# Kernel optimization log

Measured on AMD Instinct MI355X. Metric: run time of the kernel, lower is better.

The kernel has to match this reference:

```python
import jax, jax.numpy as jnp
import numpy as np

N = 100000     # nodes
H = 128        # hidden_channels == in_channels
OUT = 64       # out_channels
L = 3          # num_layers=4 -> num_layers-1 Layer modules
E = 1_600_000  # unique undirected edges (avg degree 16)
BN_EPS = 1e-5


def _make_edges():
    # Unique undirected edges, no self-loops -> dense symmetric adjacency in the
    # original module is exactly this edge set symmetrized.
    rng = np.random.default_rng(0)
    i = rng.integers(0, N, 1_700_000)
    j = rng.integers(0, N, 1_700_000)
    m = i != j
    i, j = i[m], j[m]
    lo, hi = np.minimum(i, j), np.maximum(i, j)
    pairs = np.unique(lo.astype(np.int64) * N + hi)[:E]
    lo = (pairs // N).astype(np.int32)
    hi = (pairs % N).astype(np.int32)
    src = jnp.asarray(np.concatenate([lo, hi]))  # [2E] directed
    dst = jnp.asarray(np.concatenate([hi, lo]))
    return src, dst


def setup_inputs() -> dict:
    key = jax.random.key(0)
    ks = jax.random.split(key, 24)
    nrm = lambda k, s: (jax.random.normal(k, s, dtype=jnp.float32) * 0.05)
    src, dst = _make_edges()
    return {
        "x": jax.random.normal(ks[0], (N, H), dtype=jnp.float32),
        "src": src,
        "dst": dst,
        # per-Layer MLP(in=H, hidden=H, out=H): Linear->ReLU->Linear, stacked over L
        "layer_W1": nrm(ks[1], (L, H, H)),
        "layer_b1": nrm(ks[2], (L, H)),
        "layer_W2": nrm(ks[3], (L, H, H)),
        "layer_b2": nrm(ks[4], (L, H)),
        # BatchNorm1d (eval mode: running stats)
        "bn_gamma": 1.0 + nrm(ks[5], (L, H)),
        "bn_beta": nrm(ks[6], (L, H)),
        "bn_mean": nrm(ks[7], (L, H)),
        "bn_var": jax.random.uniform(ks[8], (L, H), jnp.float32, 0.5, 1.5),
        # single shared GRUCell(H, H)
        "gru_Wih": nrm(ks[9], (3 * H, H)),
        "gru_Whh": nrm(ks[10], (3 * H, H)),
        "gru_bih": nrm(ks[11], (3 * H,)),
        "gru_bhh": nrm(ks[12], (3 * H,)),
        # mlp_last: MLP(H, H, OUT)
        "last_W1": nrm(ks[13], (H, H)),
        "last_b1": nrm(ks[14], (H,)),
        "last_W2": nrm(ks[15], (OUT, H)),
        "last_b2": nrm(ks[16], (OUT,)),
    }


def reference(x, src, dst, layer_W1, layer_b1, layer_W2, layer_b2,
              bn_gamma, bn_beta, bn_mean, bn_var,
              gru_Wih, gru_Whh, gru_bih, gru_bhh,
              last_W1, last_b1, last_W2, last_b2):
    n = x.shape[0]
    deg = jax.ops.segment_sum(jnp.ones(src.shape[0], x.dtype), dst, num_segments=n)
    inv_deg = (1.0 / jnp.maximum(deg, 1.0))[:, None]  # isolated nodes -> 0 agg
    h = jnp.zeros((n, H), x.dtype)
    for l in range(L):
        agg = jax.ops.segment_sum(x[src], dst, num_segments=n) * inv_deg  # mean over neighbors
        c = x + agg
        c = jnp.maximum(c @ layer_W1[l].T + layer_b1[l], 0.0) @ layer_W2[l].T + layer_b2[l]
        c = bn_gamma[l] * (c - bn_mean[l]) * jax.lax.rsqrt(bn_var[l] + BN_EPS) + bn_beta[l]
        # F.dropout(training=False) is identity
        gi = c @ gru_Wih.T + gru_bih  # [n, 3H]
        gh = h @ gru_Whh.T + gru_bhh
        r = jax.nn.sigmoid(gi[:, :H] + gh[:, :H])
        z = jax.nn.sigmoid(gi[:, H:2 * H] + gh[:, H:2 * H])
        nst = jnp.tanh(gi[:, 2 * H:] + r * gh[:, 2 * H:])
        h = (1.0 - z) * nst + z * h
        x = h
    return jnp.maximum(x @ last_W1.T + last_b1, 0.0) @ last_W2.T + last_b2
```

## Files before the change

### kernel.cpp

```cpp
#include <hip/hip_runtime.h>
#include <hip/hip_bf16.h>
#include <stdint.h>

typedef __bf16 bf16;
typedef __bf16 bf16x8 __attribute__((ext_vector_type(8)));
typedef float f32x4 __attribute__((ext_vector_type(4)));
typedef uint32_t u32x4 __attribute__((ext_vector_type(4)));

#define HD 128
#define LDP (HD + 8)
#define NTPB 4
#define MFMA __builtin_amdgcn_mfma_f32_16x16x32_bf16

__device__ inline float bflo(uint32_t u){ return __uint_as_float(u << 16); }
__device__ inline float bfhi(uint32_t u){ return __uint_as_float(u & 0xffff0000u); }
__device__ inline uint32_t packbf(float a, float b){
    bf16 x = (bf16)a, y = (bf16)b;
    uint16_t ux = __builtin_bit_cast(uint16_t, x), uy = __builtin_bit_cast(uint16_t, y);
    return (uint32_t)ux | ((uint32_t)uy << 16);
}
__device__ inline bf16x8 ldb8(const bf16* p){ return *(const bf16x8*)p; }
__device__ inline float sigm(float x){ return 1.f / (1.f + __expf(-x)); }
__device__ inline float tanh_fast(float x){ float t = __expf(-2.f * x); return (1.f - t) / (1.f + t); }

__global__ void k_cvt(const float* __restrict__ in, bf16* __restrict__ out, int n){
    int i = blockIdx.x * 256 + threadIdx.x;
    if (i < n) out[i] = (bf16)in[i];
}

__global__ void k_bound(const int* __restrict__ dstB, int E, int* __restrict__ rows2, int n){
    int v = blockIdx.x * 256 + threadIdx.x;
    if (v > n) return;
    int lo = 0, hi = E;
    while (lo < hi){ int mid = (lo + hi) >> 1; if (dstB[mid] < v) lo = mid + 1; else hi = mid; }
    rows2[v] = lo;
}

__global__ void k_count(const int* __restrict__ dst, int* __restrict__ deg, int ne){
    int i = blockIdx.x * 256 + threadIdx.x;
    if (i < ne) atomicAdd(&deg[dst[i]], 1);
}

__global__ void k_scan1(const int* __restrict__ deg, int* __restrict__ rows,
                        int* __restrict__ bsum, int n){
    __shared__ int lds[256];
    int b = blockIdx.x, tid = threadIdx.x;
    int i0 = b * 1024 + tid * 4;
    int v[4]; int s = 0;
#pragma unroll
    for (int j = 0; j < 4; ++j){ int idx = i0 + j; v[j] = (idx < n) ? deg[idx] : 0; s += v[j]; }
    lds[tid] = s; __syncthreads();
    int acc = s;
    for (int off = 1; off < 256; off <<= 1){
        int add = (tid >= off) ? lds[tid - off] : 0;
        __syncthreads();
        acc += add; lds[tid] = acc;
        __syncthreads();
    }
    int run = acc - s;
#pragma unroll
    for (int j = 0; j < 4; ++j){ int idx = i0 + j; if (idx < n) rows[idx] = run; run += v[j]; }
    if (tid == 255) bsum[b] = acc;
}

__global__ void k_scan2(int* __restrict__ bsum, int nb){
    __shared__ int lds[128];
    int tid = threadIdx.x;
    int v = (tid < nb) ? bsum[tid] : 0;
    lds[tid] = v; __syncthreads();
    int acc = v;
    for (int off = 1; off < 128; off <<= 1){
        int add = (tid >= off) ? lds[tid - off] : 0;
        __syncthreads();
        acc += add; lds[tid] = acc;
        __syncthreads();
    }
    if (tid < nb) bsum[tid] = acc - v;
}

__global__ void k_scan3(int* __restrict__ rows, const int* __restrict__ bsum, int n, int total){
    int i = blockIdx.x * 256 + threadIdx.x;
    if (i < n) rows[i] += bsum[i >> 10];
    if (i == n) rows[n] = total;
}

__global__ void k_fill(const int* __restrict__ src, const int* __restrict__ dst,
                       int* __restrict__ cur, int* __restrict__ col, int ne){
    int i = blockIdx.x * 256 + threadIdx.x;
    if (i < ne){ int p = atomicAdd(&cur[dst[i]], 1); col[p] = src[i]; }
}

__global__ __launch_bounds__(256) void k_gather(
    const bf16* __restrict__ curx,
    const int* __restrict__ srcB, const int* __restrict__ rows2,
    const int* __restrict__ colB, const int* __restrict__ rowsB,
    bf16* __restrict__ cout, int n)
{
    int wid = threadIdx.x >> 6, lane = threadIdx.x & 63;
    int v = blockIdx.x * 4 + wid;
    if (v >= n) return;
    int grp = lane >> 3, sl = lane & 7;
    int a0 = rows2[v], a1 = rows2[v + 1];
    int b0 = rowsB[v], b1 = rowsB[v + 1];
    int deg = (a1 - a0) + (b1 - b0);
    float inv = (deg > 0) ? 1.f / (float)deg : 0.f;

    const u32x4* base = (const u32x4*)curx;
    float acc[16];
#pragma unroll
    for (int k = 0; k < 16; ++k) acc[k] = 0.f;

    for (int j = a0 + grp; j < a1; j += 8){
        int nb = srcB[j];
        u32x4 q0 = base[(size_t)nb * 16 + sl];
        u32x4 q1 = base[(size_t)nb * 16 + 8 + sl];
#pragma unroll
        for (int k = 0; k < 4; ++k){
            acc[2*k]   += bflo(q0[k]); acc[2*k+1]   += bfhi(q0[k]);
            acc[8+2*k] += bflo(q1[k]); acc[8+2*k+1] += bfhi(q1[k]);
        }
    }
    for (int j = b0 + grp; j < b1; j += 8){
        int nb = colB[j];
        u32x4 q0 = base[(size_t)nb * 16 + sl];
        u32x4 q1 = base[(size_t)nb * 16 + 8 + sl];
#pragma unroll
        for (int k = 0; k < 4; ++k){
            acc[2*k]   += bflo(q0[k]); acc[2*k+1]   += bfhi(q0[k]);
            acc[8+2*k] += bflo(q1[k]); acc[8+2*k+1] += bfhi(q1[k]);
        }
    }
#pragma unroll
    for (int k = 0; k < 16; ++k){
        acc[k] += __shfl_xor(acc[k], 8);
        acc[k] += __shfl_xor(acc[k], 16);
        acc[k] += __shfl_xor(acc[k], 32);
    }
    if (grp == 0){
        u32x4 x0 = base[(size_t)v * 16 + sl];
        u32x4 x1 = base[(size_t)v * 16 + 8 + sl];
        u32x4 o0, o1;
#pragma unroll
        for (int k = 0; k < 4; ++k){
            o0[k] = packbf(bflo(x0[k]) + acc[2*k] * inv,   bfhi(x0[k]) + acc[2*k+1] * inv);
            o1[k] = packbf(bflo(x1[k]) + acc[8+2*k] * inv, bfhi(x1[k]) + acc[8+2*k+1] * inv);
        }
        ((u32x4*)cout)[(size_t)v * 16 + sl]     = o0;
        ((u32x4*)cout)[(size_t)v * 16 + 8 + sl] = o1;
    }
}

__global__ __launch_bounds__(256, 2) void k_layer(
    const bf16* __restrict__ cin, bf16* __restrict__ h,
    const bf16* __restrict__ W1, const float* __restrict__ b1,
    const bf16* __restrict__ W2, const float* __restrict__ b2,
    const float* __restrict__ gm, const float* __restrict__ bt,
    const float* __restrict__ mu, const float* __restrict__ vr,
    const bf16* __restrict__ Wih, const bf16* __restrict__ Whh,
    const float* __restrict__ bih, const float* __restrict__ bhh)
{
    __shared__ __align__(16) char wsm[49152];
    __shared__ __align__(16) bf16 act[4][4096];
    int wid = threadIdx.x >> 6, lane = threadIdx.x & 63;
    int r0 = blockIdx.x * 128 + wid * 32;
    int rA = lane & 15, u = lane >> 4, ko = u * 8;

    auto swz = [](uint32_t off)->uint32_t { return off ^ (((off >> 8) & 7) << 4); };
    auto gload = [&](const char* gsrc, uint32_t ldsoff){
        __builtin_amdgcn_global_load_lds(
            (const __attribute__((address_space(1))) void*)gsrc,
            (__attribute__((address_space(3))) void*)(wsm + ldsoff), 16, 0, 0);
    };
    for (int i = wid; i < 32; i += 4){
        uint32_t off = (uint32_t)i * 1024 + (uint32_t)lane * 16;
        gload((const char*)W1 + swz(off), (uint32_t)i * 1024);
    }

    bf16x8 a[2][4], ah[2][4];
#pragma unroll
    for (int m = 0; m < 2; ++m){
        const bf16* ap = cin + (size_t)(r0 + m*16 + rA) * HD + ko;
        const bf16* hp = h   + (size_t)(r0 + m*16 + rA) * HD + ko;
#pragma unroll
        for (int kk = 0; kk < 4; ++kk){ a[m][kk] = ldb8(ap + kk*32); ah[m][kk] = ldb8(hp + kk*32); }
    }

    auto ldw = [&](int slot, int kk)->bf16x8 {
        uint32_t b = (uint32_t)rA*256 + (uint32_t)u*16 + (uint32_t)kk*64;
        b ^= ((b >> 8) & 7) << 4;
        return *(const bf16x8*)(wsm + slot*4096 + b);
    };
    auto actw = [&](int r, int c, bf16 val){
        uint32_t b = (uint32_t)r*256 + (uint32_t)c*2;
        b ^= ((b >> 8) & 7) << 4;
        *(bf16*)((char*)act[wid] + b) = val;
    };
    auto actr = [&](int r, int kk)->bf16x8 {
        uint32_t b = (uint32_t)r*256 + (uint32_t)(ko + kk*32)*2;
        b ^= ((b >> 8) & 7) << 4;
        return *(const bf16x8*)((char*)act[wid] + b);
    };

    __syncthreads();

    for (int i = wid; i < 16; i += 4){
        uint32_t off = (uint32_t)i * 1024 + (uint32_t)lane * 16;
        gload((const char*)W2 + swz(off), 8*4096u + (uint32_t)i * 1024);
    }
#pragma unroll
    for (int t = 0; t < 8; ++t){
        f32x4 c0 = {0,0,0,0}, c1 = {0,0,0,0};
#pragma unroll
        for (int kk = 0; kk < 4; ++kk){
            bf16x8 wb = ldw(t, kk);
            c0 = MFMA(a[0][kk], wb, c0, 0, 0, 0);
            c1 = MFMA(a[1][kk], wb, c1, 0, 0, 0);
        }
        int c = t*16 + rA;
        float bias = b1[c];
#pragma unroll
        for (int j = 0; j < 4; ++j){
            actw(u*4 + j,      c, (bf16)fmaxf(c0[j] + bias, 0.f));
            actw(16 + u*4 + j, c, (bf16)fmaxf(c1[j] + bias, 0.f));
        }
    }
    __syncthreads();

    for (int i = wid; i < 16; i += 4){
        uint32_t off = 16384u + (uint32_t)i * 1024 + (uint32_t)lane * 16;
        gload((const char*)W2 + swz(off), (uint32_t)i * 1024);
    }
    bf16x8 a2[2][4];
#pragma unroll
    for (int m = 0; m < 2; ++m)
#pragma unroll
        for (int kk = 0; kk < 4; ++kk) a2[m][kk] = actr(m*16 + rA, kk);

    auto g2step = [&](int t, int slot){
        f32x4 c0 = {0,0,0,0}, c1 = {0,0,0,0};
#pragma unroll
        for (int kk = 0; kk < 4; ++kk){
            bf16x8 wb = ldw(slot, kk);
            c0 = MFMA(a2[0][kk], wb, c0, 0, 0, 0);
            c1 = MFMA(a2[1][kk], wb, c1, 0, 0, 0);
        }
        int c = t*16 + rA;
        float s = gm[c] * rsqrtf(vr[c] + 1e-5f);
        float o = bt[c] - mu[c] * s;
        float bias = b2[c];
#pragma unroll
        for (int j = 0; j < 4; ++j){
            actw(u*4 + j,      c, (bf16)((c0[j] + bias) * s + o));
            actw(16 + u*4 + j, c, (bf16)((c1[j] + bias) * s + o));
        }
    };
#pragma unroll
    for (int t = 0; t < 4; ++t) g2step(t, 8 + t);
    __syncthreads();

    auto stageGRU = [&](int t){
        uint32_t sb = (t & 1) ? 10u : 4u;
        for (int i = wid; i < 24; i += 4){
            int p = i >> 2, s = i & 3;
            int g = p >> 1, m = p & 1;
            const char* Wsrc = (const char*)(m ? Whh : Wih) + (size_t)g*32768 + (size_t)t*4096;
            uint32_t slot = sb + (uint32_t)p; if (slot >= 12) slot -= 12;
            uint32_t off = (uint32_t)s * 1024 + (uint32_t)lane * 16;
            gload(Wsrc + swz(off), slot*4096 + (uint32_t)s * 1024);
        }
    };
    stageGRU(0);
#pragma unroll
    for (int t = 4; t < 8; ++t) g2step(t, t - 4);
    __syncthreads();

    bf16x8 ac[2][4];
#pragma unroll
    for (int m = 0; m < 2; ++m)
#pragma unroll
        for (int kk = 0; kk < 4; ++kk) ac[m][kk] = actr(m*16 + rA, kk);

#pragma unroll
    for (int t = 0; t < 8; ++t){
        if (t < 7) stageGRU(t + 1);
        uint32_t sb = (t & 1) ? 10u : 4u;
        int s0 = sb, s1 = sb+1, s2 = sb+2, s3 = sb+3, s4 = sb+4, s5 = sb+5;
        if (s2 >= 12) s2 -= 12; if (s3 >= 12) s3 -= 12;
        if (s4 >= 12) s4 -= 12; if (s5 >= 12) s5 -= 12;
        if (s1 >= 12) s1 -= 12;
        int c = t*16 + rA;
        float hold[8];
#pragma unroll
        for (int j = 0; j < 4; ++j){
            hold[j]   = (float)h[(size_t)(r0 + u*4 + j) * HD + c];
            hold[4+j] = (float)h[(size_t)(r0 + 16 + u*4 + j) * HD + c];
        }
        f32x4 rr0={0,0,0,0}, rr1={0,0,0,0}, zz0={0,0,0,0}, zz1={0,0,0,0};
        f32x4 gi0={0,0,0,0}, gi1={0,0,0,0}, gh0={0,0,0,0}, gh1={0,0,0,0};
#pragma unroll
        for (int kk = 0; kk < 4; ++kk){
            bf16x8 Bri = ldw(s0, kk), Brh = ldw(s1, kk);
            bf16x8 Bzi = ldw(s2, kk), Bzh = ldw(s3, kk);
            bf16x8 Bni = ldw(s4, kk), Bnh = ldw(s5, kk);
            rr0 = MFMA(ac[0][kk], Bri, rr0, 0, 0, 0);
            rr1 = MFMA(ac[1][kk], Bri, rr1, 0, 0, 0);
            rr0 = MFMA(ah[0][kk], Brh, rr0, 0, 0, 0);
            rr1 = MFMA(ah[1][kk], Brh, rr1, 0, 0, 0);
            zz0 = MFMA(ac[0][kk], Bzi, zz0, 0, 0, 0);
            zz1 = MFMA(ac[1][kk], Bzi, zz1, 0, 0, 0);
            zz0 = MFMA(ah[0][kk], Bzh, zz0, 0, 0, 0);
            zz1 = MFMA(ah[1][kk], Bzh, zz1, 0, 0, 0);
            gi0 = MFMA(ac[0][kk], Bni, gi0, 0, 0, 0);
            gi1 = MFMA(ac[1][kk], Bni, gi1, 0, 0, 0);
            gh0 = MFMA(ah[0][kk], Bnh, gh0, 0, 0, 0);
            gh1 = MFMA(ah[1][kk], Bnh, gh1, 0, 0, 0);
        }
        float br = bih[c] + bhh[c];
        float bz = bih[c + 128] + bhh[c + 128];
        float bin = bih[c + 256], bhn = bhh[c + 256];
#pragma unroll
        for (int j = 0; j < 4; ++j){
            size_t i0 = (size_t)(r0 + u*4 + j) * HD + c;
            size_t i1 = (size_t)(r0 + 16 + u*4 + j) * HD + c;
            float rg0 = sigm(rr0[j] + br), rg1 = sigm(rr1[j] + br);
            float zg0 = sigm(zz0[j] + bz), zg1 = sigm(zz1[j] + bz);
            float ng0 = tanh_fast(gi0[j] + bin + rg0 * (gh0[j] + bhn));
            float ng1 = tanh_fast(gi1[j] + bin + rg1 * (gh1[j] + bhn));
            h[i0] = (bf16)((1.f - zg0) * ng0 + zg0 * hold[j]);
            h[i1] = (bf16)((1.f - zg1) * ng1 + zg1 * hold[4+j]);
        }
        __syncthreads();
    }
}

__global__ __launch_bounds__(256) void k_final(
    const bf16* __restrict__ hin, const bf16* __restrict__ W1, const float* __restrict__ b1,
    const bf16* __restrict__ W2, const float* __restrict__ b2,
    float* __restrict__ out, int nTiles)
{
    __shared__ bf16 lds[NTPB][16][LDP];
    int wid = threadIdx.x >> 6, lane = threadIdx.x & 63;
    int tile = blockIdx.x * NTPB + wid;
    if (tile >= nTiles) return;
    int r0 = tile * 16;
    int rA = lane & 15, u = lane >> 4, ko = u * 8;

    bf16x8 a[4];
    const bf16* ap = hin + (size_t)(r0 + rA) * HD + ko;
#pragma unroll
    for (int kk = 0; kk < 4; ++kk) a[kk] = ldb8(ap + kk * 32);

#pragma unroll
    for (int t = 0; t < 8; ++t){
        f32x4 acc = {0.f, 0.f, 0.f, 0.f};
        int c = t * 16 + rA;
        const bf16* bp = W1 + (size_t)c * HD + ko;
#pragma unroll
        for (int kk = 0; kk < 4; ++kk)
            acc = MFMA(a[kk], ldb8(bp + kk * 32), acc, 0, 0, 0);
        float bias = b1[c];
#pragma unroll
        for (int j = 0; j < 4; ++j){
            float v = fmaxf(acc[j] + bias, 0.f);
            lds[wid][u * 4 + j][c] = (bf16)v;
        }
    }
    __threadfence_block();
    bf16x8 a2[4];
    const bf16* lp = &lds[wid][rA][ko];
#pragma unroll
    for (int kk = 0; kk < 4; ++kk) a2[kk] = ldb8(lp + kk * 32);

#pragma unroll
    for (int t = 0; t < 4; ++t){
        f32x4 acc = {0.f, 0.f, 0.f, 0.f};
        int c = t * 16 + rA;
        const bf16* bp = W2 + (size_t)c * HD + ko;
#pragma unroll
        for (int kk = 0; kk < 4; ++kk)
            acc = MFMA(a2[kk], ldb8(bp + kk * 32), acc, 0, 0, 0);
        float bias = b2[c];
#pragma unroll
        for (int j = 0; j < 4; ++j)
            out[(size_t)(r0 + u * 4 + j) * 64 + c] = acc[j] + bias;
    }
}

extern "C" void kernel_launch(void* const* d_in, const int* in_sizes, int n_in,
                              void* d_out, int out_size, void* d_ws, size_t ws_size,
                              hipStream_t stream)
{
    const float* x    = (const float*)d_in[0];
    const int*   src  = (const int*)d_in[1];
    const int*   dst  = (const int*)d_in[2];
    const float* lW1  = (const float*)d_in[3];
    const float* lb1  = (const float*)d_in[4];
    const float* lW2  = (const float*)d_in[5];
    const float* lb2  = (const float*)d_in[6];
    const float* gmm  = (const float*)d_in[7];
    const float* bta  = (const float*)d_in[8];
    const float* mun  = (const float*)d_in[9];
    const float* vrr  = (const float*)d_in[10];
    const float* Wih  = (const float*)d_in[11];
    const float* Whh  = (const float*)d_in[12];
    const float* bih  = (const float*)d_in[13];
    const float* bhh  = (const float*)d_in[14];
    const float* fW1  = (const float*)d_in[15];
    const float* fb1  = (const float*)d_in[16];
    const float* fW2  = (const float*)d_in[17];
    const float* fb2  = (const float*)d_in[18];

    int n  = in_sizes[0] / HD;
    int ne = in_sizes[1];
    int E  = ne / 2;
    int L  = in_sizes[3] / (HD * HD);
    int nPad = (n + 127) & ~127;

    char* w = (char*)d_ws;
    auto alloc = [&](size_t bytes) -> char* {
        char* p = w; w += (bytes + 255) & ~(size_t)255; return p;
    };
    bf16* xbf  = (bf16*)alloc((size_t)nPad * HD * 2);
    bf16* hbf  = (bf16*)alloc((size_t)nPad * HD * 2);
    bf16* cin  = (bf16*)alloc((size_t)nPad * HD * 2);
    bf16* W1b  = (bf16*)alloc((size_t)L * HD * HD * 2);
    bf16* W2b  = (bf16*)alloc((size_t)L * HD * HD * 2);
    bf16* Wib  = (bf16*)alloc((size_t)3 * HD * HD * 2);
    bf16* Whb  = (bf16*)alloc((size_t)3 * HD * HD * 2);
    bf16* fW1b = (bf16*)alloc((size_t)HD * HD * 2);
    bf16* fW2b = (bf16*)alloc((size_t)64 * HD * 2);
    int*  degB = (int*)alloc((size_t)n * 4);
    int*  rowsB= (int*)alloc((size_t)(n + 1) * 4);
    int*  rows2= (int*)alloc((size_t)(n + 1) * 4);
    int*  bsum = (int*)alloc(512);
    int*  curB = (int*)alloc((size_t)n * 4);
    int*  colB = (int*)alloc((size_t)E * 4);

    auto cvt = [&](const float* i, bf16* o, int cnt){
        k_cvt<<<(cnt + 255) / 256, 256, 0, stream>>>(i, o, cnt);
    };
    cvt(x,   xbf,  n * HD);
    cvt(lW1, W1b,  L * HD * HD);
    cvt(lW2, W2b,  L * HD * HD);
    cvt(Wih, Wib,  3 * HD * HD);
    cvt(Whh, Whb,  3 * HD * HD);
    cvt(fW1, fW1b, HD * HD);
    cvt(fW2, fW2b, 64 * HD);

    hipMemsetAsync(degB, 0, (size_t)n * 4, stream);
    hipMemsetAsync(hbf, 0, (size_t)nPad * HD * 2, stream);

    k_bound<<<(n + 1 + 255) / 256, 256, 0, stream>>>(dst + E, E, rows2, n);
    k_count<<<(E + 255) / 256, 256, 0, stream>>>(dst, degB, E);
    int nb = (n + 1023) / 1024;
    k_scan1<<<nb, 256, 0, stream>>>(degB, rowsB, bsum, n);
    k_scan2<<<1, 128, 0, stream>>>(bsum, nb);
    k_scan3<<<(n + 1 + 255) / 256, 256, 0, stream>>>(rowsB, bsum, n, E);
    hipMemcpyAsync(curB, rowsB, (size_t)n * 4, hipMemcpyDeviceToDevice, stream);
    k_fill<<<(E + 255) / 256, 256, 0, stream>>>(src, dst, curB, colB, E);

    int gL = nPad / 128;
    int nT16 = (n + 15) / 16;
    int gF = (nT16 + NTPB - 1) / NTPB;

    const bf16* curp = xbf;
    for (int l = 0; l < L; ++l){
        k_gather<<<(n + 3) / 4, 256, 0, stream>>>(curp, src + E, rows2, colB, rowsB, cin, n);
        k_layer<<<gL, 256, 0, stream>>>(cin, hbf,
            W1b + (size_t)l * HD * HD, lb1 + l * HD,
            W2b + (size_t)l * HD * HD, lb2 + l * HD,
            gmm + l * HD, bta + l * HD, mun + l * HD, vrr + l * HD,
            Wib, Whb, bih, bhh);
        curp = hbf;
    }
    k_final<<<gF, 256, 0, stream>>>(hbf, fW1b, fb1, fW2b, fb2, (float*)d_out, nT16);
}
```

Baseline: 819.7 us.

## Split fused layer kernel into persistent MLP and column-split GRU kernels

After: 1.076 ms. +31.3%, slower.

```diff
diff --git a/kernel.cpp b/kernel.cpp
--- a/kernel.cpp
+++ b/kernel.cpp
@@ -22,6 +22,7 @@
 __device__ inline bf16x8 ldb8(const bf16* p){ return *(const bf16x8*)p; }
 __device__ inline float sigm(float x){ return 1.f / (1.f + __expf(-x)); }
 __device__ inline float tanh_fast(float x){ float t = __expf(-2.f * x); return (1.f - t) / (1.f + t); }
+__device__ inline uint32_t swz(uint32_t b){ return b ^ (((b >> 8) & 7u) << 4); }
 
 __global__ void k_cvt(const float* __restrict__ in, bf16* __restrict__ out, int n){
     int i = blockIdx.x * 256 + threadIdx.x;
@@ -150,186 +151,165 @@
     }
 }
 
-__global__ __launch_bounds__(256, 2) void k_layer(
-    const bf16* __restrict__ cin, bf16* __restrict__ h,
-    const bf16* __restrict__ W1, const float* __restrict__ b1,
-    const bf16* __restrict__ W2, const float* __restrict__ b2,
+__global__ __launch_bounds__(512, 2) void k_mlp(
+    bf16* __restrict__ cio,
+    const bf16* __restrict__ W1g, const float* __restrict__ b1,
+    const bf16* __restrict__ W2g, const float* __restrict__ b2,
     const float* __restrict__ gm, const float* __restrict__ bt,
-    const float* __restrict__ mu, const float* __restrict__ vr,
+    const float* __restrict__ mu, const float* __restrict__ vr, int nT128)
+{
+    __shared__ __align__(16) char wsm[65536];
+    __shared__ __align__(16) char actm[32768];
+    int tid = threadIdx.x, wid = tid >> 6, lane = tid & 63;
+    int rA = lane & 15, u = lane >> 4, ko = u * 8;
+
+#pragma unroll
+    for (int i = 0; i < 8; ++i){
+        int c = i * 8 + wid;
+        uint32_t o = (uint32_t)c * 1024;
+        const char* base = (c < 32) ? (const char*)W1g : (const char*)W2g;
+        uint32_t po = (o & 32767u) + (uint32_t)lane * 16;
+        __builtin_amdgcn_global_load_lds(
+            (const __attribute__((address_space(1))) void*)(base + swz(po)),
+            (__attribute__((address_space(3))) void*)(wsm + o), 16, 0, 0);
+    }
+    __syncthreads();
+
+    char* act = actm + wid * 4096;
+    auto ldw = [&](uint32_t regionOff, int t, int kk)->bf16x8 {
+        uint32_t b = regionOff + (uint32_t)(t*16 + rA)*256 + (uint32_t)u*16 + (uint32_t)kk*64;
+        return *(const bf16x8*)(wsm + swz(b));
+    };
+    auto actw = [&](int r, int c, bf16 val){
+        uint32_t b = (uint32_t)r*256 + (uint32_t)c*2;
+        *(bf16*)(act + swz(b)) = val;
+    };
+    auto actr = [&](int r, int kk)->bf16x8 {
+        uint32_t b = (uint32_t)r*256 + (uint32_t)(ko + kk*32)*2;
+        return *(const bf16x8*)(act + swz(b));
+    };
+
+    for (int t = blockIdx.x; t < nT128; t += gridDim.x){
+        int r0 = t * 128 + wid * 16;
+        bf16x8 a[4];
+        const bf16* ap = cio + (size_t)(r0 + rA) * HD + ko;
+#pragma unroll
+        for (int kk = 0; kk < 4; ++kk) a[kk] = ldb8(ap + kk * 32);
+
+#pragma unroll
+        for (int tt = 0; tt < 8; ++tt){
+            f32x4 acc = {0,0,0,0};
+#pragma unroll
+            for (int kk = 0; kk < 4; ++kk)
+                acc = MFMA(a[kk], ldw(0, tt, kk), acc, 0, 0, 0);
+            int c = tt*16 + rA;
+            float bias = b1[c];
+#pragma unroll
+            for (int j = 0; j < 4; ++j)
+                actw(u*4 + j, c, (bf16)fmaxf(acc[j] + bias, 0.f));
+        }
+        __threadfence_block();
+        bf16x8 a2[4];
+#pragma unroll
+        for (int kk = 0; kk < 4; ++kk) a2[kk] = actr(rA, kk);
+
+#pragma unroll
+        for (int tt = 0; tt < 8; ++tt){
+            f32x4 acc = {0,0,0,0};
+#pragma unroll
+            for (int kk = 0; kk < 4; ++kk)
+                acc = MFMA(a2[kk], ldw(32768u, tt, kk), acc, 0, 0, 0);
+            int c = tt*16 + rA;
+            float s = gm[c] * rsqrtf(vr[c] + 1e-5f);
+            float o = bt[c] - mu[c] * s;
+            float bias = b2[c];
+#pragma unroll
+            for (int j = 0; j < 4; ++j)
+                cio[(size_t)(r0 + u*4 + j) * HD + c] = (bf16)((acc[j] + bias) * s + o);
+        }
+        __threadfence_block();
+    }
+}
+
+__global__ __launch_bounds__(256, 3) void k_gru(
+    const bf16* __restrict__ cbn, const bf16* __restrict__ hOld, bf16* __restrict__ hNew,
     const bf16* __restrict__ Wih, const bf16* __restrict__ Whh,
-    const float* __restrict__ bih, const float* __restrict__ bhh)
+    const float* __restrict__ bih, const float* __restrict__ bhh, int nT128)
 {
     __shared__ __align__(16) char wsm[49152];
-    __shared__ __align__(16) bf16 act[4][4096];
-    int wid = threadIdx.x >> 6, lane = threadIdx.x & 63;
-    int r0 = blockIdx.x * 128 + wid * 32;
+    int tid = threadIdx.x, wid = tid >> 6, lane = tid & 63;
+    int ug = blockIdx.x & 3;
     int rA = lane & 15, u = lane >> 4, ko = u * 8;
 
-    auto swz = [](uint32_t off)->uint32_t { return off ^ (((off >> 8) & 7) << 4); };
-    auto gload = [&](const char* gsrc, uint32_t ldsoff){
+#pragma unroll
+    for (int i = 0; i < 12; ++i){
+        int c = i * 4 + wid;
+        uint32_t o = (uint32_t)c * 1024;
+        int p = o >> 13;
+        int g = p >> 1, m = p & 1;
+        const char* base = (const char*)(m ? Whh : Wih) + ((size_t)(g * 128 + ug * 32)) * 256;
+        uint32_t po = (o & 8191u) + (uint32_t)lane * 16;
         __builtin_amdgcn_global_load_lds(
-            (const __attribute__((address_space(1))) void*)gsrc,
-            (__attribute__((address_space(3))) void*)(wsm + ldsoff), 16, 0, 0);
-    };
-    for (int i = wid; i < 32; i += 4){
-        uint32_t off = (uint32_t)i * 1024 + (uint32_t)lane * 16;
-        gload((const char*)W1 + swz(off), (uint32_t)i * 1024);
-    }
-
-    bf16x8 a[2][4], ah[2][4];
-#pragma unroll
-    for (int m = 0; m < 2; ++m){
-        const bf16* ap = cin + (size_t)(r0 + m*16 + rA) * HD + ko;
-        const bf16* hp = h   + (size_t)(r0 + m*16 + rA) * HD + ko;
-#pragma unroll
-        for (int kk = 0; kk < 4; ++kk){ a[m][kk] = ldb8(ap + kk*32); ah[m][kk] = ldb8(hp + kk*32); }
-    }
-
-    auto ldw = [&](int slot, int kk)->bf16x8 {
-        uint32_t b = (uint32_t)rA*256 + (uint32_t)u*16 + (uint32_t)kk*64;
-        b ^= ((b >> 8) & 7) << 4;
-        return *(const bf16x8*)(wsm + slot*4096 + b);
-    };
-    auto actw = [&](int r, int c, bf16 val){
-        uint32_t b = (uint32_t)r*256 + (uint32_t)c*2;
-        b ^= ((b >> 8) & 7) << 4;
-        *(bf16*)((char*)act[wid] + b) = val;
-    };
-    auto actr = [&](int r, int kk)->bf16x8 {
-        uint32_t b = (uint32_t)r*256 + (uint32_t)(ko + kk*32)*2;
-        b ^= ((b >> 8) & 7) << 4;
-        return *(const bf16x8*)((char*)act[wid] + b);
-    };
-
+            (const __attribute__((address_space(1))) void*)(base + swz(po)),
+            (__attribute__((address_space(3))) void*)(wsm + o), 16, 0, 0);
+    }
     __syncthreads();
 
-    for (int i = wid; i < 16; i += 4){
-        uint32_t off = (uint32_t)i * 1024 + (uint32_t)lane * 16;
-        gload((const char*)W2 + swz(off), 8*4096u + (uint32_t)i * 1024);
-    }
-#pragma unroll
-    for (int t = 0; t < 8; ++t){
-        f32x4 c0 = {0,0,0,0}, c1 = {0,0,0,0};
-#pragma unroll
-        for (int kk = 0; kk < 4; ++kk){
-            bf16x8 wb = ldw(t, kk);
-            c0 = MFMA(a[0][kk], wb, c0, 0, 0, 0);
-            c1 = MFMA(a[1][kk], wb, c1, 0, 0, 0);
-        }
-        int c = t*16 + rA;
-        float bias = b1[c];
-#pragma unroll
-        for (int j = 0; j < 4; ++j){
-            actw(u*4 + j,      c, (bf16)fmaxf(c0[j] + bias, 0.f));
-            actw(16 + u*4 + j, c, (bf16)fmaxf(c1[j] + bias, 0.f));
-        }
-    }
-    __syncthreads();
-
-    for (int i = wid; i < 16; i += 4){
-        uint32_t off = 16384u + (uint32_t)i * 1024 + (uint32_t)lane * 16;
-        gload((const char*)W2 + swz(off), (uint32_t)i * 1024);
-    }
-    bf16x8 a2[2][4];
-#pragma unroll
-    for (int m = 0; m < 2; ++m)
-#pragma unroll
-        for (int kk = 0; kk < 4; ++kk) a2[m][kk] = actr(m*16 + rA, kk);
-
-    auto g2step = [&](int t, int slot){
-        f32x4 c0 = {0,0,0,0}, c1 = {0,0,0,0};
-#pragma unroll
-        for (int kk = 0; kk < 4; ++kk){
-            bf16x8 wb = ldw(slot, kk);
-            c0 = MFMA(a2[0][kk], wb, c0, 0, 0, 0);
-            c1 = MFMA(a2[1][kk], wb, c1, 0, 0, 0);
-        }
-        int c = t*16 + rA;
-        float s = gm[c] * rsqrtf(vr[c] + 1e-5f);
-        float o = bt[c] - mu[c] * s;
-        float bias = b2[c];
-#pragma unroll
-        for (int j = 0; j < 4; ++j){
-            actw(u*4 + j,      c, (bf16)((c0[j] + bias) * s + o));
-            actw(16 + u*4 + j, c, (bf16)((c1[j] + bias) * s + o));
-        }
-    };
-#pragma unroll
-    for (int t = 0; t < 4; ++t) g2step(t, 8 + t);
-    __syncthreads();
-
-    auto stageGRU = [&](int t){
-        uint32_t sb = (t & 1) ? 10u : 4u;
-        for (int i = wid; i < 24; i += 4){
-            int p = i >> 2, s = i & 3;
-            int g = p >> 1, m = p & 1;
-            const char* Wsrc = (const char*)(m ? Whh : Wih) + (size_t)g*32768 + (size_t)t*4096;
-            uint32_t slot = sb + (uint32_t)p; if (slot >= 12) slot -= 12;
-            uint32_t off = (uint32_t)s * 1024 + (uint32_t)lane * 16;
-            gload(Wsrc + swz(off), slot*4096 + (uint32_t)s * 1024);
-        }
-    };
-    stageGRU(0);
-#pragma unroll
-    for (int t = 4; t < 8; ++t) g2step(t, t - 4);
-    __syncthreads();
-
-    bf16x8 ac[2][4];
-#pragma unroll
-    for (int m = 0; m < 2; ++m)
-#pragma unroll
-        for (int kk = 0; kk < 4; ++kk) ac[m][kk] = actr(m*16 + rA, kk);
-
-#pragma unroll
-    for (int t = 0; t < 8; ++t){
-        if (t < 7) stageGRU(t + 1);
-        uint32_t sb = (t & 1) ? 10u : 4u;
-        int s0 = sb, s1 = sb+1, s2 = sb+2, s3 = sb+3, s4 = sb+4, s5 = sb+5;
-        if (s2 >= 12) s2 -= 12; if (s3 >= 12) s3 -= 12;
-        if (s4 >= 12) s4 -= 12; if (s5 >= 12) s5 -= 12;
-        if (s1 >= 12) s1 -= 12;
-        int c = t*16 + rA;
-        float hold[8];
-#pragma unroll
-        for (int j = 0; j < 4; ++j){
-            hold[j]   = (float)h[(size_t)(r0 + u*4 + j) * HD + c];
-            hold[4+j] = (float)h[(size_t)(r0 + 16 + u*4 + j) * HD + c];
-        }
-        f32x4 rr0={0,0,0,0}, rr1={0,0,0,0}, zz0={0,0,0,0}, zz1={0,0,0,0};
-        f32x4 gi0={0,0,0,0}, gi1={0,0,0,0}, gh0={0,0,0,0}, gh1={0,0,0,0};
-#pragma unroll
-        for (int kk = 0; kk < 4; ++kk){
-            bf16x8 Bri = ldw(s0, kk), Brh = ldw(s1, kk);
-            bf16x8 Bzi = ldw(s2, kk), Bzh = ldw(s3, kk);
-            bf16x8 Bni = ldw(s4, kk), Bnh = ldw(s5, kk);
-            rr0 = MFMA(ac[0][kk], Bri, rr0, 0, 0, 0);
-            rr1 = MFMA(ac[1][kk], Bri, rr1, 0, 0, 0);
-            rr0 = MFMA(ah[0][kk], Brh, rr0, 0, 0, 0);
-            rr1 = MFMA(ah[1][kk], Brh, rr1, 0, 0, 0);
-            zz0 = MFMA(ac[0][kk], Bzi, zz0, 0, 0, 0);
-            zz1 = MFMA(ac[1][kk], Bzi, zz1, 0, 0, 0);
-            zz0 = MFMA(ah[0][kk], Bzh, zz0, 0, 0, 0);
-            zz1 = MFMA(ah[1][kk], Bzh, zz1, 0, 0, 0);
-            gi0 = MFMA(ac[0][kk], Bni, gi0, 0, 0, 0);
-            gi1 = MFMA(ac[1][kk], Bni, gi1, 0, 0, 0);
-            gh0 = MFMA(ah[0][kk], Bnh, gh0, 0, 0, 0);
-            gh1 = MFMA(ah[1][kk], Bnh, gh1, 0, 0, 0);
-        }
-        float br = bih[c] + bhh[c];
-        float bz = bih[c + 128] + bhh[c + 128];
-        float bin = bih[c + 256], bhn = bhh[c + 256];
-#pragma unroll
-        for (int j = 0; j < 4; ++j){
-            size_t i0 = (size_t)(r0 + u*4 + j) * HD + c;
-            size_t i1 = (size_t)(r0 + 16 + u*4 + j) * HD + c;
-            float rg0 = sigm(rr0[j] + br), rg1 = sigm(rr1[j] + br);
-            float zg0 = sigm(zz0[j] + bz), zg1 = sigm(zz1[j] + bz);
-            float ng0 = tanh_fast(gi0[j] + bin + rg0 * (gh0[j] + bhn));
-            float ng1 = tanh_fast(gi1[j] + bin + rg1 * (gh1[j] + bhn));
-            h[i0] = (bf16)((1.f - zg0) * ng0 + zg0 * hold[j]);
-            h[i1] = (bf16)((1.f - zg1) * ng1 + zg1 * hold[4+j]);
-        }
-        __syncthreads();
+    auto ldw = [&](int p, int ct, int kk)->bf16x8 {
+        uint32_t b = (uint32_t)p*8192 + (uint32_t)(ct*16 + rA)*256 + (uint32_t)u*16 + (uint32_t)kk*64;
+        return *(const bf16x8*)(wsm + swz(b));
+    };
+
+    int nB = (int)(gridDim.x >> 2);
+    for (int t = (int)(blockIdx.x >> 2); t < nT128; t += nB){
+        int r0 = t * 128 + wid * 32;
+        bf16x8 ac[2][4], ah[2][4];
+#pragma unroll
+        for (int m = 0; m < 2; ++m){
+            const bf16* cp = cbn  + (size_t)(r0 + m*16 + rA) * HD + ko;
+            const bf16* hp = hOld + (size_t)(r0 + m*16 + rA) * HD + ko;
+#pragma unroll
+            for (int kk = 0; kk < 4; ++kk){ ac[m][kk] = ldb8(cp + kk*32); ah[m][kk] = ldb8(hp + kk*32); }
+        }
+#pragma unroll
+        for (int ct = 0; ct < 2; ++ct){
+            f32x4 rr0={0,0,0,0}, rr1={0,0,0,0}, zz0={0,0,0,0}, zz1={0,0,0,0};
+            f32x4 gi0={0,0,0,0}, gi1={0,0,0,0}, gh0={0,0,0,0}, gh1={0,0,0,0};
+#pragma unroll
+            for (int kk = 0; kk < 4; ++kk){
+                bf16x8 Bri = ldw(0, ct, kk), Brh = ldw(1, ct, kk);
+                bf16x8 Bzi = ldw(2, ct, kk), Bzh = ldw(3, ct, kk);
+                bf16x8 Bni = ldw(4, ct, kk), Bnh = ldw(5, ct, kk);
+                rr0 = MFMA(ac[0][kk], Bri, rr0, 0, 0, 0);
+                rr1 = MFMA(ac[1][kk], Bri, rr1, 0, 0, 0);
+                rr0 = MFMA(ah[0][kk], Brh, rr0, 0, 0, 0);
+                rr1 = MFMA(ah[1][kk], Brh, rr1, 0, 0, 0);
+                zz0 = MFMA(ac[0][kk], Bzi, zz0, 0, 0, 0);
+                zz1 = MFMA(ac[1][kk], Bzi, zz1, 0, 0, 0);
+                zz0 = MFMA(ah[0][kk], Bzh, zz0, 0, 0, 0);
+                zz1 = MFMA(ah[1][kk], Bzh, zz1, 0, 0, 0);
+                gi0 = MFMA(ac[0][kk], Bni, gi0, 0, 0, 0);
+                gi1 = MFMA(ac[1][kk], Bni, gi1, 0, 0, 0);
+                gh0 = MFMA(ah[0][kk], Bnh, gh0, 0, 0, 0);
+                gh1 = MFMA(ah[1][kk], Bnh, gh1, 0, 0, 0);
+            }
+            int c = ug * 32 + ct * 16 + rA;
+            float br = bih[c] + bhh[c];
+            float bz = bih[c + 128] + bhh[c + 128];
+            float bin = bih[c + 256], bhn = bhh[c + 256];
+#pragma unroll
+            for (int j = 0; j < 4; ++j){
+                size_t i0 = (size_t)(r0 + u*4 + j) * HD + c;
+                size_t i1 = (size_t)(r0 + 16 + u*4 + j) * HD + c;
+                float h0 = (float)hOld[i0], h1 = (float)hOld[i1];
+                float rg0 = sigm(rr0[j] + br), rg1 = sigm(rr1[j] + br);
+                float zg0 = sigm(zz0[j] + bz), zg1 = sigm(zz1[j] + bz);
+                float ng0 = tanh_fast(gi0[j] + bin + rg0 * (gh0[j] + bhn));
+                float ng1 = tanh_fast(gi1[j] + bin + rg1 * (gh1[j] + bhn));
+                hNew[i0] = (bf16)((1.f - zg0) * ng0 + zg0 * h0);
+                hNew[i1] = (bf16)((1.f - zg1) * ng1 + zg1 * h1);
+            }
+        }
     }
 }
 
@@ -421,7 +401,8 @@
         char* p = w; w += (bytes + 255) & ~(size_t)255; return p;
     };
     bf16* xbf  = (bf16*)alloc((size_t)nPad * HD * 2);
-    bf16* hbf  = (bf16*)alloc((size_t)nPad * HD * 2);
+    bf16* hA   = (bf16*)alloc((size_t)nPad * HD * 2);
+    bf16* hB   = (bf16*)alloc((size_t)nPad * HD * 2);
     bf16* cin  = (bf16*)alloc((size_t)nPad * HD * 2);
     bf16* W1b  = (bf16*)alloc((size_t)L * HD * HD * 2);
     bf16* W2b  = (bf16*)alloc((size_t)L * HD * HD * 2);
@@ -448,7 +429,7 @@
     cvt(fW2, fW2b, 64 * HD);
 
     hipMemsetAsync(degB, 0, (size_t)n * 4, stream);
-    hipMemsetAsync(hbf, 0, (size_t)nPad * HD * 2, stream);
+    hipMemsetAsync(hA, 0, (size_t)nPad * HD * 2, stream);
 
     k_bound<<<(n + 1 + 255) / 256, 256, 0, stream>>>(dst + E, E, rows2, n);
     k_count<<<(E + 255) / 256, 256, 0, stream>>>(dst, degB, E);
@@ -459,19 +440,20 @@
     hipMemcpyAsync(curB, rowsB, (size_t)n * 4, hipMemcpyDeviceToDevice, stream);
     k_fill<<<(E + 255) / 256, 256, 0, stream>>>(src, dst, curB, colB, E);
 
-    int gL = nPad / 128;
+    int nT128 = nPad / 128;
     int nT16 = (n + 15) / 16;
     int gF = (nT16 + NTPB - 1) / NTPB;
 
     const bf16* curp = xbf;
     for (int l = 0; l < L; ++l){
         k_gather<<<(n + 3) / 4, 256, 0, stream>>>(curp, src + E, rows2, colB, rowsB, cin, n);
-        k_layer<<<gL, 256, 0, stream>>>(cin, hbf,
+        k_mlp<<<256, 512, 0, stream>>>(cin,
             W1b + (size_t)l * HD * HD, lb1 + l * HD,
             W2b + (size_t)l * HD * HD, lb2 + l * HD,
-            gmm + l * HD, bta + l * HD, mun + l * HD, vrr + l * HD,
-            Wib, Whb, bih, bhh);
-        curp = hbf;
-    }
-    k_final<<<gF, 256, 0, stream>>>(hbf, fW1b, fb1, fW2b, fb2, (float*)d_out, nT16);
-}
+            gmm + l * HD, bta + l * HD, mun + l * HD, vrr + l * HD, nT128);
+        k_gru<<<768, 256, 0, stream>>>(cin, hA, hB, Wib, Whb, bih, bhh, nT128);
+        bf16* tmp = hA; hA = hB; hB = tmp;
+        curp = hA;
+    }
+    k_final<<<gF, 256, 0, stream>>>(hA, fW1b, fb1, fW2b, fb2, (float*)d_out, nT16);
+}
```
